# Kernel optimization log

Hardware: AMD Instinct MI355X
Metric: run time of the kernel (lower is better)

Reference implementation:

```python
import jax, jax.numpy as jnp
import numpy as np

H = 1024      # hidden_size
I = 2048      # expert intermediate_size (SwiGLU)
E = 8         # num_local_experts
B, S = 2, 4096
EPS = 1e-5
INIT = 0.02


def setup_inputs() -> dict:
    key = jax.random.key(0)
    ks = jax.random.split(key, 9)
    return {
        "hidden_states": jax.random.normal(ks[0], (B, S, H), jnp.float32),
        "ln_w": jnp.ones((H,), jnp.float32),
        "ln_b": jnp.zeros((H,), jnp.float32),
        "router_w": jax.random.normal(ks[1], (H, E), jnp.float32) * INIT,
        "gate_w": jax.random.normal(ks[2], (E, H, I), jnp.float32) * INIT,
        "up_w": jax.random.normal(ks[3], (E, H, I), jnp.float32) * INIT,
        "down_w": jax.random.normal(ks[4], (E, I, H), jnp.float32) * INIT,
        "sh_gate": jax.random.normal(ks[5], (H, I), jnp.float32) * INIT,
        "sh_up": jax.random.normal(ks[6], (H, I), jnp.float32) * INIT,
        "sh_down": jax.random.normal(ks[7], (I, H), jnp.float32) * INIT,
    }


def _layernorm(x, w, b):
    mu = jnp.mean(x, axis=-1, keepdims=True)
    var = jnp.mean(jnp.square(x - mu), axis=-1, keepdims=True)
    return (x - mu) * jax.lax.rsqrt(var + EPS) * w + b


def reference(hidden_states, ln_w, ln_b, router_w, gate_w, up_w, down_w,
              sh_gate, sh_up, sh_down):
    b, s, h = hidden_states.shape
    normed = _layernorm(hidden_states, ln_w, ln_b)
    xf = normed.reshape(-1, h)                       # [T, H]

    # Router: top-1 expert per token, sigmoid gating (Llama-4 style)
    logits = xf @ router_w                           # [T, E]
    top_idx = jnp.argmax(logits, axis=-1)            # [T]
    top_score = jax.nn.sigmoid(jnp.max(logits, axis=-1))  # [T]

    # Routed experts: scan over experts, mask+scale tokens assigned to each.
    def body(acc, ew):
        g, u, d, e = ew
        w = jnp.where(top_idx == e, top_score, 0.0)[:, None]  # [T, 1]
        xe = xf * w                                            # gate score applied to input
        hmid = jax.nn.silu(xe @ g) * (xe @ u)                  # [T, I]
        return acc + hmid @ d, None

    routed, _ = jax.lax.scan(
        body, jnp.zeros_like(xf), (gate_w, up_w, down_w, jnp.arange(E)))

    # Shared expert (dense SwiGLU) applied to all tokens
    shared = (jax.nn.silu(xf @ sh_gate) * (xf @ sh_up)) @ sh_down  # [T, H]

    moe_out = (routed + shared).reshape(b, s, h)
    return hidden_states + moe_out
```

## Files before the change

kernel.cpp:

```cpp
#include <hip/hip_runtime.h>

typedef unsigned short ushort_t;
typedef unsigned int uint_t;

#define T_TOK 8192
#define HDIM 1024
#define IDIM 2048
#define NEXP 8
#define RPAD_MAX 10240
#define TOTROWS (RPAD_MAX + T_TOK)

using f32x4 = __attribute__((ext_vector_type(4))) float;
using s16x8 = __attribute__((ext_vector_type(8))) short;

#define SBAR() do { asm volatile("" ::: "memory"); __builtin_amdgcn_s_barrier(); asm volatile("" ::: "memory"); } while (0)
#define VMW(n) asm volatile("s_waitcnt vmcnt(" #n ")" ::: "memory")
#define LGKM(n) do { asm volatile("s_waitcnt lgkmcnt(" #n ")" ::: "memory"); __builtin_amdgcn_sched_barrier(0); } while (0)

__device__ __forceinline__ float b2f(ushort_t h) {
    return __uint_as_float(((uint_t)h) << 16);
}
__device__ __forceinline__ ushort_t f2bf(float f) {
    uint_t u = __float_as_uint(f);
    uint_t r = (u + 0x7FFFu + ((u >> 16) & 1u)) >> 16;
    return (ushort_t)r;
}
__device__ __forceinline__ void gload16(const void* g, void* l) {
    __builtin_amdgcn_global_load_lds(
        (const __attribute__((address_space(1))) void*)g,
        (__attribute__((address_space(3))) void*)l, 16, 0, 0);
}
__device__ __forceinline__ void gdec(int gi, int& r, int& kg) {
    int prow = gi >> 3, v = (gi & 7) ^ (prow & 7);
    r = 2 * prow + (v >> 2);
    kg = v & 3;
}
__device__ __forceinline__ void sbmap(int bid, int SBC, int NSB, int& rt, int& ct) {
    int x = bid & 7, j = bid >> 3;
    int r = j >> 5, pos = j & 31;
    int sb = r * 8 + x;
    int rem = NSB - r * 8;
    if (rem < 8) {
        int share = 8 / rem;
        int cap = 32 / share;
        sb = r * 8 + x / share;
        pos = (x % share) * cap + (pos % cap);
    }
    int sbr = sb / SBC, sbc = sb % SBC;
    rt = sbr * 4 + (pos >> 3);
    ct = sbc * 8 + (pos & 7);
}

__global__ void tcvt64(const float* __restrict__ gw, const float* __restrict__ shg,
                       const float* __restrict__ uw, const float* __restrict__ shu,
                       const float* __restrict__ dw, const float* __restrict__ shd,
                       ushort_t* __restrict__ gwt, ushort_t* __restrict__ uwt,
                       ushort_t* __restrict__ dwt) {
    __shared__ float tile[64][65];
    int z = blockIdx.z;
    const float* src;
    ushort_t* dst;
    int R, C, bx = blockIdx.x, by = blockIdx.y;
    if (z < 18) {
        int zz = z % 9;
        R = HDIM; C = IDIM;
        if (z < 9) { src = zz < 8 ? gw + (size_t)zz * HDIM * IDIM : shg; dst = gwt + (size_t)zz * IDIM * HDIM; }
        else       { src = zz < 8 ? uw + (size_t)zz * HDIM * IDIM : shu; dst = uwt + (size_t)zz * IDIM * HDIM; }
    } else {
        int zz = z - 18;
        R = IDIM; C = HDIM;
        src = zz < 8 ? dw + (size_t)zz * IDIM * HDIM : shd;
        dst = dwt + (size_t)zz * HDIM * IDIM;
        int t = bx; bx = by; by = t;
    }
    int c0 = bx * 64, r0 = by * 64;
    int tx = threadIdx.x, ty = threadIdx.y;
#pragma unroll
    for (int i = 0; i < 16; ++i)
        tile[ty + i * 4][tx] = src[(size_t)(r0 + ty + i * 4) * C + c0 + tx];
    __syncthreads();
    int tid = ty * 64 + tx;
    int rr = (tid & 15) * 4, cc0 = tid >> 4;
#pragma unroll
    for (int it = 0; it < 4; ++it) {
        int c = cc0 + it * 16;
        ushort4 v;
        v.x = f2bf(tile[rr + 0][c]);
        v.y = f2bf(tile[rr + 1][c]);
        v.z = f2bf(tile[rr + 2][c]);
        v.w = f2bf(tile[rr + 3][c]);
        *(ushort4*)&dst[(size_t)(c0 + c) * R + r0 + rr] = v;
    }
}

__global__ void ln_router(const float* __restrict__ x, const float* __restrict__ lnw,
                          const float* __restrict__ lnb, const float* __restrict__ rw,
                          ushort_t* __restrict__ normed, int* __restrict__ top_idx,
                          float* __restrict__ top_score, int* __restrict__ cnt) {
    int t = blockIdx.x, tid = threadIdx.x;
    const float* xr = x + (size_t)t * HDIM;
    float v[4];
    float s = 0.f, ss = 0.f;
#pragma unroll
    for (int i = 0; i < 4; i++) {
        v[i] = xr[tid + i * 256];
        s += v[i];
        ss += v[i] * v[i];
    }
#pragma unroll
    for (int o = 32; o; o >>= 1) {
        s += __shfl_down(s, o);
        ss += __shfl_down(ss, o);
    }
    __shared__ float rs_[4], rss_[4], stats[2];
    int wid = tid >> 6, lane = tid & 63;
    if (!lane) { rs_[wid] = s; rss_[wid] = ss; }
    __syncthreads();
    if (!tid) {
        float S = rs_[0] + rs_[1] + rs_[2] + rs_[3];
        float SS = rss_[0] + rss_[1] + rss_[2] + rss_[3];
        float mu = S * (1.f / HDIM);
        float var = SS * (1.f / HDIM) - mu * mu;
        stats[0] = mu;
        stats[1] = rsqrtf(var + 1e-5f);
    }
    __syncthreads();
    float mu = stats[0], rsg = stats[1];
    float lg[8] = {0, 0, 0, 0, 0, 0, 0, 0};
#pragma unroll
    for (int i = 0; i < 4; i++) {
        int h = tid + i * 256;
        float xn = (v[i] - mu) * rsg * lnw[h] + lnb[h];
        normed[(size_t)t * HDIM + h] = f2bf(xn);
        const float* rwh = rw + (size_t)h * NEXP;
#pragma unroll
        for (int e = 0; e < 8; e++) lg[e] += xn * rwh[e];
    }
#pragma unroll
    for (int o = 32; o; o >>= 1)
#pragma unroll
        for (int e = 0; e < 8; e++) lg[e] += __shfl_down(lg[e], o);
    __shared__ float lred[4][8];
    if (!lane)
#pragma unroll
        for (int e = 0; e < 8; e++) lred[wid][e] = lg[e];
    __syncthreads();
    if (!tid) {
        float best = -1e30f;
        int bi = 0;
#pragma unroll
        for (int e = 0; e < 8; e++) {
            float L = lred[0][e] + lred[1][e] + lred[2][e] + lred[3][e];
            if (L > best) { best = L; bi = e; }
        }
        top_idx[t] = bi;
        top_score[t] = 1.f / (1.f + __expf(-best));
        atomicAdd(&cnt[bi], 1);
    }
}

__global__ void scan_k(const int* __restrict__ cnt, int* __restrict__ pad_off,
                       int* __restrict__ fill) {
    if (threadIdx.x == 0) {
        int o = 0;
        for (int e = 0; e < NEXP; e++) {
            pad_off[e] = o;
            o += (cnt[e] + 255) & ~255;
        }
        pad_off[NEXP] = o;
    }
    if (threadIdx.x < NEXP) fill[threadIdx.x] = 0;
}

__global__ void scatter_k(const ushort_t* __restrict__ normed, const int* __restrict__ top_idx,
                          const float* __restrict__ top_score, const int* __restrict__ pad_off,
                          int* __restrict__ fill, int* __restrict__ order,
                          ushort_t* __restrict__ xs) {
    int t = blockIdx.x, tid = threadIdx.x;
    __shared__ int spos;
    if (!tid) {
        int e = top_idx[t];
        int p = pad_off[e] + atomicAdd(&fill[e], 1);
        order[p] = t;
        spos = p;
    }
    __syncthreads();
    int pos = spos;
    float sc = top_score[t];
    const ushort4* src = (const ushort4*)(normed + (size_t)t * HDIM);
    ushort4* dst = (ushort4*)(xs + (size_t)pos * HDIM);
    ushort4 a = src[tid];
    a.x = f2bf(b2f(a.x) * sc);
    a.y = f2bf(b2f(a.y) * sc);
    a.z = f2bf(b2f(a.z) * sc);
    a.w = f2bf(b2f(a.w) * sc);
    dst[tid] = a;
}

__global__ __launch_bounds__(512, 2) void gemm1_k(
    const ushort_t* __restrict__ X, const ushort_t* __restrict__ Wg,
    const ushort_t* __restrict__ Wu, const int* __restrict__ pad_off,
    ushort_t* __restrict__ hmid) {
    __shared__ __align__(16) ushort_t lds[4 * 16384];
    const int CT = IDIM / 128;
    const int NH = HDIM / 32;
    int rt, ct;
    sbmap(blockIdx.x, CT / 8, (TOTROWS / 256 / 4) * (CT / 8), rt, ct);
    int row0 = rt * 256, col0 = ct * 128;
    int e;
    if (row0 >= RPAD_MAX) e = 8;
    else {
        if (row0 >= pad_off[NEXP]) return;
        e = 0;
        while (e < 7 && row0 >= pad_off[e + 1]) ++e;
    }
    const ushort_t* wgp = Wg + (size_t)e * IDIM * HDIM;
    const ushort_t* wup = Wu + (size_t)e * IDIM * HDIM;

    const int tid = threadIdx.x, l = tid & 63, w = tid >> 6;
    const int wm = w >> 2, wn = w & 3;
    const int lr = l & 15, lg4 = l >> 4;

    int rA0, kA0, rA1, kA1, rB, kB;
    gdec(tid, rA0, kA0);
    gdec(512 + tid, rA1, kA1);
    gdec(tid, rB, kB);
    const ushort_t* srcA0 = X + (size_t)(row0 + rA0) * HDIM + kA0 * 8;
    const ushort_t* srcA1 = X + (size_t)(row0 + rA1) * HDIM + kA1 * 8;
    const ushort_t* srcBg = wgp + (size_t)(col0 + rB) * HDIM + kB * 8;
    const ushort_t* srcBu = wup + (size_t)(col0 + rB) * HDIM + kB * 8;
    const int dA0 = tid * 8, dA1 = (512 + tid) * 8, dB = tid * 8;

    const int s_slot = (((l & 1) << 2) | lg4) ^ ((l >> 1) & 7);
    const int aoff = (wm * 64 + (lr >> 1)) * 64 + s_slot * 8;
    const int boff = (wn * 16 + (lr >> 1)) * 64 + s_slot * 8;

    f32x4 accg[8][2] = {};
    f32x4 accu[8][2] = {};

#define G1_STAGE(h) do { int ko = (h) * 32; int hb_ = ((h) & 3) * 16384;       \
        gload16(srcA0 + ko, &lds[hb_ + dA0]);                                  \
        gload16(srcA1 + ko, &lds[hb_ + dA1]);                                  \
        gload16(srcBg + ko, &lds[hb_ + 8192 + dB]);                            \
        gload16(srcBu + ko, &lds[hb_ + 12288 + dB]); } while (0)

#define G1_PH(h, VMWAIT, DOSTAGE) do {                                         \
        const int hb = ((h) & 3) * 16384;                                      \
        s16x8 av[8], bv[4];                                                    \
        _Pragma("unroll")                                                      \
        for (int i = 0; i < 4; ++i) av[i] = *(const s16x8*)&lds[hb + aoff + i * 512]; \
        _Pragma("unroll")                                                      \
        for (int i = 0; i < 2; ++i) bv[i] = *(const s16x8*)&lds[hb + 8192 + boff + i * 512]; \
        _Pragma("unroll")                                                      \
        for (int i = 0; i < 2; ++i) bv[2 + i] = *(const s16x8*)&lds[hb + 12288 + boff + i * 512]; \
        _Pragma("unroll")                                                      \
        for (int i = 0; i < 4; ++i) av[4 + i] = *(const s16x8*)&lds[hb + aoff + 2048 + i * 512]; \
        if (DOSTAGE) G1_STAGE((h) + 3);                                        \
        VMWAIT;                                                                \
        SBAR();                                                                \
        LGKM(4);                                                               \
        __builtin_amdgcn_s_setprio(1);                                         \
        _Pragma("unroll")                                                      \
        for (int m = 0; m < 4; ++m) {                                          \
            accg[m][0] = __builtin_amdgcn_mfma_f32_16x16x32_bf16(av[m], bv[0], accg[m][0], 0, 0, 0); \
            accg[m][1] = __builtin_amdgcn_mfma_f32_16x16x32_bf16(av[m], bv[1], accg[m][1], 0, 0, 0); \
            accu[m][0] = __builtin_amdgcn_mfma_f32_16x16x32_bf16(av[m], bv[2], accu[m][0], 0, 0, 0); \
            accu[m][1] = __builtin_amdgcn_mfma_f32_16x16x32_bf16(av[m], bv[3], accu[m][1], 0, 0, 0); \
        }                                                                      \
        __builtin_amdgcn_s_setprio(0);                                         \
        LGKM(0);                                                               \
        __builtin_amdgcn_s_setprio(1);                                         \
        _Pragma("unroll")                                                      \
        for (int m = 0; m < 4; ++m) {                                          \
            accg[4 + m][0] = __builtin_amdgcn_mfma_f32_16x16x32_bf16(av[4 + m], bv[0], accg[4 + m][0], 0, 0, 0); \
            accg[4 + m][1] = __builtin_amdgcn_mfma_f32_16x16x32_bf16(av[4 + m], bv[1], accg[4 + m][1], 0, 0, 0); \
            accu[4 + m][0] = __builtin_amdgcn_mfma_f32_16x16x32_bf16(av[4 + m], bv[2], accu[4 + m][0], 0, 0, 0); \
            accu[4 + m][1] = __builtin_amdgcn_mfma_f32_16x16x32_bf16(av[4 + m], bv[3], accu[4 + m][1], 0, 0, 0); \
        }                                                                      \
        __builtin_amdgcn_s_setprio(0);                                         \
        SBAR();                                                                \
    } while (0)

    G1_STAGE(0);
    G1_STAGE(1);
    G1_STAGE(2);
    VMW(8);
    SBAR();
    for (int h = 0; h < NH - 3; ++h) G1_PH(h, VMW(8), 1);
    G1_PH(NH - 3, VMW(4), 0);
    G1_PH(NH - 2, VMW(0), 0);
    G1_PH(NH - 1, VMW(0), 0);

#pragma unroll
    for (int mf = 0; mf < 8; ++mf) {
        int row = row0 + wm * 128 + mf * 16 + lg4 * 4;
#pragma unroll
        for (int nf = 0; nf < 2; ++nf) {
            int col = col0 + wn * 32 + nf * 16 + lr;
#pragma unroll
            for (int rr = 0; rr < 4; ++rr) {
                float g = accg[mf][nf][rr], u = accu[mf][nf][rr];
                float val = g / (1.f + __expf(-g)) * u;
                hmid[(size_t)(row + rr) * IDIM + col] = f2bf(val);
            }
        }
    }
#undef G1_STAGE
#undef G1_PH
}

template <int SHARED>
__global__ __launch_bounds__(512, 2) void gemm2_k(
    const ushort_t* __restrict__ Hm, const ushort_t* __restrict__ Wd,
    const int* __restrict__ pad_off, const int* __restrict__ order,
    const float* __restrict__ hs, float* __restrict__ out, int RT) {
    __shared__ __align__(16) ushort_t lds[4 * 12288];
    const int CT = HDIM / 128;
    const int NH = IDIM / 32;
    int rt, ct;
    sbmap(blockIdx.x, 1, RT / 4, rt, ct);
    int row0 = rt * 256, col0 = ct * 128;
    const ushort_t* wdp;
    if (SHARED) {
        wdp = Wd + (size_t)8 * HDIM * IDIM;
    } else {
        if (row0 >= pad_off[NEXP]) return;
        int e = 0;
        while (e < 7 && row0 >= pad_off[e + 1]) ++e;
        wdp = Wd + (size_t)e * HDIM * IDIM;
    }
    const int tid = threadIdx.x, l = tid & 63, w = tid >> 6;
    const int wm = w >> 1, wn = w & 1;
    const int lr = l & 15, lg4 = l >> 4;

    int rA0, kA0, rA1, kA1, rB, kB;
    gdec(tid, rA0, kA0);
    gdec(512 + tid, rA1, kA1);
    gdec(tid, rB, kB);
    const ushort_t* srcA0 = Hm + (size_t)(row0 + rA0) * IDIM + kA0 * 8;
    const ushort_t* srcA1 = Hm + (size_t)(row0 + rA1) * IDIM + kA1 * 8;
    const ushort_t* srcB = wdp + (size_t)(col0 + rB) * IDIM + kB * 8;
    const int dA0 = tid * 8, dA1 = (512 + tid) * 8, dB = tid * 8;

    const int s_slot = (((l & 1) << 2) | lg4) ^ ((l >> 1) & 7);
    const int aoff = (wm * 32 + (lr >> 1)) * 64 + s_slot * 8;
    const int boff = (wn * 32 + (lr >> 1)) * 64 + s_slot * 8;

    f32x4 acc[4][4] = {};

#define G2_STAGE(h) do { int ko = (h) * 32; int hb_ = ((h) & 3) * 12288;       \
        gload16(srcA0 + ko, &lds[hb_ + dA0]);                                  \
        gload16(srcA1 + ko, &lds[hb_ + dA1]);                                  \
        gload16(srcB + ko, &lds[hb_ + 8192 + dB]); } while (0)

#define G2_PH(h, VMWAIT, DOSTAGE) do {                                         \
        const int hb = ((h) & 3) * 12288;                                      \
        s16x8 av[4], bv[4];                                                    \
        _Pragma("unroll")                                                      \
        for (int i = 0; i < 4; ++i) av[i] = *(const s16x8*)&lds[hb + aoff + i * 512]; \
        _Pragma("unroll")                                                      \
        for (int i = 0; i < 4; ++i) bv[i] = *(const s16x8*)&lds[hb + 8192 + boff + i * 512]; \
        if (DOSTAGE) G2_STAGE((h) + 3);                                        \
        VMWAIT;                                                                \
        SBAR();                                                                \
        LGKM(0);                                                               \
        __builtin_amdgcn_s_setprio(1);                                         \
        _Pragma("unroll")                                                      \
        for (int m = 0; m < 4; ++m)                                            \
            _Pragma("unroll")                                                  \
            for (int n = 0; n < 4; ++n)                                        \
                acc[m][n] = __builtin_amdgcn_mfma_f32_16x16x32_bf16(av[m], bv[n], acc[m][n], 0, 0, 0); \
        __builtin_amdgcn_s_setprio(0);                                         \
        SBAR();                                                                \
    } while (0)

    G2_STAGE(0);
    G2_STAGE(1);
    G2_STAGE(2);
    VMW(6);
    SBAR();
    for (int h = 0; h < NH - 3; ++h) G2_PH(h, VMW(6), 1);
    G2_PH(NH - 3, VMW(3), 0);
    G2_PH(NH - 2, VMW(0), 0);
    G2_PH(NH - 1, VMW(0), 0);

#pragma unroll
    for (int mf = 0; mf < 4; ++mf) {
        int row = row0 + wm * 64 + mf * 16 + lg4 * 4;
#pragma unroll
        for (int nf = 0; nf < 4; ++nf) {
            int col = col0 + wn * 64 + nf * 16 + lr;
#pragma unroll
            for (int rr = 0; rr < 4; ++rr) {
                int rw_ = row + rr;
                if (SHARED) {
                    size_t o = (size_t)rw_ * HDIM + col;
                    out[o] += hs[o] + acc[mf][nf][rr];
                } else {
                    int tok = order[rw_];
                    if (tok >= 0) {
                        size_t o = (size_t)tok * HDIM + col;
                        out[o] = acc[mf][nf][rr];
                    }
                }
            }
        }
    }
#undef G2_STAGE
#undef G2_PH
}

extern "C" void kernel_launch(void* const* d_in, const int* in_sizes, int n_in,
                              void* d_out, int out_size, void* d_ws, size_t ws_size,
                              hipStream_t stream) {
    const float* hs = (const float*)d_in[0];
    const float* lnw = (const float*)d_in[1];
    const float* lnb = (const float*)d_in[2];
    const float* rw = (const float*)d_in[3];
    const float* gw = (const float*)d_in[4];
    const float* uw = (const float*)d_in[5];
    const float* dw = (const float*)d_in[6];
    const float* shg = (const float*)d_in[7];
    const float* shu = (const float*)d_in[8];
    const float* shd = (const float*)d_in[9];
    float* out = (float*)d_out;

    char* p = (char*)d_ws;
    auto alloc = [&](size_t bytes) {
        void* r = (void*)p;
        p += (bytes + 255) & ~(size_t)255;
        return r;
    };
    ushort_t* xsbuf = (ushort_t*)alloc((size_t)TOTROWS * HDIM * 2);
    ushort_t* hmid = (ushort_t*)alloc((size_t)TOTROWS * IDIM * 2);
    ushort_t* gwt = (ushort_t*)alloc((size_t)9 * IDIM * HDIM * 2);
    ushort_t* uwt = (ushort_t*)alloc((size_t)9 * IDIM * HDIM * 2);
    ushort_t* dwt = (ushort_t*)alloc((size_t)9 * HDIM * IDIM * 2);
    int* cnt = (int*)alloc(NEXP * 4);
    int* pad_off = (int*)alloc((NEXP + 1) * 4);
    int* fill = (int*)alloc(NEXP * 4);
    int* top_idx = (int*)alloc(T_TOK * 4);
    float* top_sc = (float*)alloc(T_TOK * 4);
    int* order = (int*)alloc(RPAD_MAX * 4);

    ushort_t* normed = xsbuf + (size_t)RPAD_MAX * HDIM;

    hipMemsetAsync(cnt, 0, NEXP * 4, stream);
    hipMemsetAsync(order, 0xFF, RPAD_MAX * 4, stream);
    hipMemsetAsync(xsbuf, 0, (size_t)RPAD_MAX * HDIM * 2, stream);

    tcvt64<<<dim3(IDIM / 64, HDIM / 64, 27), dim3(64, 4), 0, stream>>>(
        gw, shg, uw, shu, dw, shd, gwt, uwt, dwt);

    ln_router<<<T_TOK, 256, 0, stream>>>(hs, lnw, lnb, rw, normed, top_idx, top_sc, cnt);
    scan_k<<<1, 64, 0, stream>>>(cnt, pad_off, fill);
    scatter_k<<<T_TOK, 256, 0, stream>>>(normed, top_idx, top_sc, pad_off, fill, order, xsbuf);

    {
        int RT = TOTROWS / 256, CT = IDIM / 128;
        gemm1_k<<<RT * CT, 512, 0, stream>>>(xsbuf, gwt, uwt, pad_off, hmid);
    }
    {
        int RT = RPAD_MAX / 256;
        gemm2_k<0><<<RT * (HDIM / 128), 512, 0, stream>>>(
            hmid, dwt, pad_off, order, hs, out, RT);
    }
    {
        int RT = T_TOK / 256;
        gemm2_k<1><<<RT * (HDIM / 128), 512, 0, stream>>>(
            hmid + (size_t)RPAD_MAX * IDIM, dwt, pad_off, order, hs, out, RT);
    }
}
```

Baseline: 577.6 us.

## Switch expert GEMMs to BK=64 double-buffered LDS pipeline

```diff
diff --git a/kernel.cpp b/kernel.cpp
--- a/kernel.cpp
+++ b/kernel.cpp
@@ -16,6 +16,7 @@
 #define SBAR() do { asm volatile("" ::: "memory"); __builtin_amdgcn_s_barrier(); asm volatile("" ::: "memory"); } while (0)
 #define VMW(n) asm volatile("s_waitcnt vmcnt(" #n ")" ::: "memory")
 #define LGKM(n) do { asm volatile("s_waitcnt lgkmcnt(" #n ")" ::: "memory"); __builtin_amdgcn_sched_barrier(0); } while (0)
+#define SCHB() __builtin_amdgcn_sched_barrier(0)
 
 __device__ __forceinline__ float b2f(ushort_t h) {
     return __uint_as_float(((uint_t)h) << 16);
@@ -29,11 +30,6 @@
     __builtin_amdgcn_global_load_lds(
         (const __attribute__((address_space(1))) void*)g,
         (__attribute__((address_space(3))) void*)l, 16, 0, 0);
-}
-__device__ __forceinline__ void gdec(int gi, int& r, int& kg) {
-    int prow = gi >> 3, v = (gi & 7) ^ (prow & 7);
-    r = 2 * prow + (v >> 2);
-    kg = v & 3;
 }
 __device__ __forceinline__ void sbmap(int bid, int SBC, int NSB, int& rt, int& ct) {
     int x = bid & 7, j = bid >> 3;
@@ -201,9 +197,9 @@
     const ushort_t* __restrict__ X, const ushort_t* __restrict__ Wg,
     const ushort_t* __restrict__ Wu, const int* __restrict__ pad_off,
     ushort_t* __restrict__ hmid) {
-    __shared__ __align__(16) ushort_t lds[4 * 16384];
+    __shared__ __align__(16) ushort_t lds[2 * 32768];
     const int CT = IDIM / 128;
-    const int NH = HDIM / 32;
+    const int NH = HDIM / 64;
     int rt, ct;
     sbmap(blockIdx.x, CT / 8, (TOTROWS / 256 / 4) * (CT / 8), rt, ct);
     int row0 = rt * 256, col0 = ct * 128;
@@ -221,75 +217,85 @@
     const int wm = w >> 2, wn = w & 3;
     const int lr = l & 15, lg4 = l >> 4;
 
-    int rA0, kA0, rA1, kA1, rB, kB;
-    gdec(tid, rA0, kA0);
-    gdec(512 + tid, rA1, kA1);
-    gdec(tid, rB, kB);
-    const ushort_t* srcA0 = X + (size_t)(row0 + rA0) * HDIM + kA0 * 8;
-    const ushort_t* srcA1 = X + (size_t)(row0 + rA1) * HDIM + kA1 * 8;
-    const ushort_t* srcBg = wgp + (size_t)(col0 + rB) * HDIM + kB * 8;
-    const ushort_t* srcBu = wup + (size_t)(col0 + rB) * HDIM + kB * 8;
-    const int dA0 = tid * 8, dA1 = (512 + tid) * 8, dB = tid * 8;
-
-    const int s_slot = (((l & 1) << 2) | lg4) ^ ((l >> 1) & 7);
-    const int aoff = (wm * 64 + (lr >> 1)) * 64 + s_slot * 8;
-    const int boff = (wn * 16 + (lr >> 1)) * 64 + s_slot * 8;
+    const ushort_t* sA[4];
+#pragma unroll
+    for (int j = 0; j < 4; ++j) {
+        int gi = tid + j * 512, row = gi >> 3, kg = (gi & 7) ^ (row & 7);
+        sA[j] = X + (size_t)(row0 + row) * HDIM + kg * 8;
+    }
+    const ushort_t *sBg[2], *sBu[2];
+#pragma unroll
+    for (int j = 0; j < 2; ++j) {
+        int gi = tid + j * 512, row = gi >> 3, kg = (gi & 7) ^ (row & 7);
+        sBg[j] = wgp + (size_t)(col0 + row) * HDIM + kg * 8;
+        sBu[j] = wup + (size_t)(col0 + row) * HDIM + kg * 8;
+    }
+    const int sl0 = (lg4 ^ (lr & 7)) * 8, sl1 = ((4 + lg4) ^ (lr & 7)) * 8;
+    const int aob = (wm * 128 + lr) * 64;
+    const int bob = (wn * 32 + lr) * 64;
 
     f32x4 accg[8][2] = {};
     f32x4 accu[8][2] = {};
 
-#define G1_STAGE(h) do { int ko = (h) * 32; int hb_ = ((h) & 3) * 16384;       \
-        gload16(srcA0 + ko, &lds[hb_ + dA0]);                                  \
-        gload16(srcA1 + ko, &lds[hb_ + dA1]);                                  \
-        gload16(srcBg + ko, &lds[hb_ + 8192 + dB]);                            \
-        gload16(srcBu + ko, &lds[hb_ + 12288 + dB]); } while (0)
-
-#define G1_PH(h, VMWAIT, DOSTAGE) do {                                         \
-        const int hb = ((h) & 3) * 16384;                                      \
-        s16x8 av[8], bv[4];                                                    \
-        _Pragma("unroll")                                                      \
-        for (int i = 0; i < 4; ++i) av[i] = *(const s16x8*)&lds[hb + aoff + i * 512]; \
-        _Pragma("unroll")                                                      \
-        for (int i = 0; i < 2; ++i) bv[i] = *(const s16x8*)&lds[hb + 8192 + boff + i * 512]; \
-        _Pragma("unroll")                                                      \
-        for (int i = 0; i < 2; ++i) bv[2 + i] = *(const s16x8*)&lds[hb + 12288 + boff + i * 512]; \
-        _Pragma("unroll")                                                      \
-        for (int i = 0; i < 4; ++i) av[4 + i] = *(const s16x8*)&lds[hb + aoff + 2048 + i * 512]; \
-        if (DOSTAGE) G1_STAGE((h) + 3);                                        \
-        VMWAIT;                                                                \
-        SBAR();                                                                \
-        LGKM(4);                                                               \
+#define G1_STAGE(h) do { int ko = (h) * 64; int hb_ = ((h) & 1) * 32768;       \
+        gload16(sA[0] + ko, &lds[hb_ + tid * 8]);                              \
+        gload16(sA[1] + ko, &lds[hb_ + 4096 + tid * 8]);                       \
+        gload16(sA[2] + ko, &lds[hb_ + 8192 + tid * 8]);                       \
+        gload16(sA[3] + ko, &lds[hb_ + 12288 + tid * 8]);                      \
+        gload16(sBg[0] + ko, &lds[hb_ + 16384 + tid * 8]);                     \
+        gload16(sBg[1] + ko, &lds[hb_ + 20480 + tid * 8]);                     \
+        gload16(sBu[0] + ko, &lds[hb_ + 24576 + tid * 8]);                     \
+        gload16(sBu[1] + ko, &lds[hb_ + 28672 + tid * 8]); } while (0)
+
+#define G1_PH(h, DOSTAGE) do {                                                 \
+        const int hb = ((h) & 1) * 32768;                                      \
+        s16x8 a0[8], a1[8], b0[4], b1[4];                                      \
+        _Pragma("unroll")                                                      \
+        for (int m = 0; m < 8; ++m) a0[m] = *(const s16x8*)&lds[hb + aob + m * 1024 + sl0]; \
+        _Pragma("unroll")                                                      \
+        for (int n = 0; n < 2; ++n) {                                          \
+            b0[n] = *(const s16x8*)&lds[hb + 16384 + bob + n * 1024 + sl0];    \
+            b0[2 + n] = *(const s16x8*)&lds[hb + 24576 + bob + n * 1024 + sl0]; \
+        }                                                                      \
+        SCHB();                                                                \
+        _Pragma("unroll")                                                      \
+        for (int m = 0; m < 8; ++m) a1[m] = *(const s16x8*)&lds[hb + aob + m * 1024 + sl1]; \
+        _Pragma("unroll")                                                      \
+        for (int n = 0; n < 2; ++n) {                                          \
+            b1[n] = *(const s16x8*)&lds[hb + 16384 + bob + n * 1024 + sl1];    \
+            b1[2 + n] = *(const s16x8*)&lds[hb + 24576 + bob + n * 1024 + sl1]; \
+        }                                                                      \
+        SCHB();                                                                \
+        if (DOSTAGE) G1_STAGE((h) + 1);                                        \
+        LGKM(12);                                                              \
         __builtin_amdgcn_s_setprio(1);                                         \
         _Pragma("unroll")                                                      \
-        for (int m = 0; m < 4; ++m) {                                          \
-            accg[m][0] = __builtin_amdgcn_mfma_f32_16x16x32_bf16(av[m], bv[0], accg[m][0], 0, 0, 0); \
-            accg[m][1] = __builtin_amdgcn_mfma_f32_16x16x32_bf16(av[m], bv[1], accg[m][1], 0, 0, 0); \
-            accu[m][0] = __builtin_amdgcn_mfma_f32_16x16x32_bf16(av[m], bv[2], accu[m][0], 0, 0, 0); \
-            accu[m][1] = __builtin_amdgcn_mfma_f32_16x16x32_bf16(av[m], bv[3], accu[m][1], 0, 0, 0); \
+        for (int m = 0; m < 8; ++m) {                                          \
+            accg[m][0] = __builtin_amdgcn_mfma_f32_16x16x32_bf16(a0[m], b0[0], accg[m][0], 0, 0, 0); \
+            accg[m][1] = __builtin_amdgcn_mfma_f32_16x16x32_bf16(a0[m], b0[1], accg[m][1], 0, 0, 0); \
+            accu[m][0] = __builtin_amdgcn_mfma_f32_16x16x32_bf16(a0[m], b0[2], accu[m][0], 0, 0, 0); \
+            accu[m][1] = __builtin_amdgcn_mfma_f32_16x16x32_bf16(a0[m], b0[3], accu[m][1], 0, 0, 0); \
         }                                                                      \
         __builtin_amdgcn_s_setprio(0);                                         \
         LGKM(0);                                                               \
         __builtin_amdgcn_s_setprio(1);                                         \
         _Pragma("unroll")                                                      \
-        for (int m = 0; m < 4; ++m) {                                          \
-            accg[4 + m][0] = __builtin_amdgcn_mfma_f32_16x16x32_bf16(av[4 + m], bv[0], accg[4 + m][0], 0, 0, 0); \
-            accg[4 + m][1] = __builtin_amdgcn_mfma_f32_16x16x32_bf16(av[4 + m], bv[1], accg[4 + m][1], 0, 0, 0); \
-            accu[4 + m][0] = __builtin_amdgcn_mfma_f32_16x16x32_bf16(av[4 + m], bv[2], accu[4 + m][0], 0, 0, 0); \
-            accu[4 + m][1] = __builtin_amdgcn_mfma_f32_16x16x32_bf16(av[4 + m], bv[3], accu[4 + m][1], 0, 0, 0); \
+        for (int m = 0; m < 8; ++m) {                                          \
+            accg[m][0] = __builtin_amdgcn_mfma_f32_16x16x32_bf16(a1[m], b1[0], accg[m][0], 0, 0, 0); \
+            accg[m][1] = __builtin_amdgcn_mfma_f32_16x16x32_bf16(a1[m], b1[1], accg[m][1], 0, 0, 0); \
+            accu[m][0] = __builtin_amdgcn_mfma_f32_16x16x32_bf16(a1[m], b1[2], accu[m][0], 0, 0, 0); \
+            accu[m][1] = __builtin_amdgcn_mfma_f32_16x16x32_bf16(a1[m], b1[3], accu[m][1], 0, 0, 0); \
         }                                                                      \
         __builtin_amdgcn_s_setprio(0);                                         \
+        VMW(0);                                                                \
         SBAR();                                                                \
     } while (0)
 
     G1_STAGE(0);
-    G1_STAGE(1);
-    G1_STAGE(2);
-    VMW(8);
+    VMW(0);
     SBAR();
-    for (int h = 0; h < NH - 3; ++h) G1_PH(h, VMW(8), 1);
-    G1_PH(NH - 3, VMW(4), 0);
-    G1_PH(NH - 2, VMW(0), 0);
-    G1_PH(NH - 1, VMW(0), 0);
+    for (int h = 0; h < NH - 1; ++h) G1_PH(h, 1);
+    G1_PH(NH - 1, 0);
 
 #pragma unroll
     for (int mf = 0; mf < 8; ++mf) {
@@ -314,9 +320,8 @@
     const ushort_t* __restrict__ Hm, const ushort_t* __restrict__ Wd,
     const int* __restrict__ pad_off, const int* __restrict__ order,
     const float* __restrict__ hs, float* __restrict__ out, int RT) {
-    __shared__ __align__(16) ushort_t lds[4 * 12288];
-    const int CT = HDIM / 128;
-    const int NH = IDIM / 32;
+    __shared__ __align__(16) ushort_t lds[2 * 24576];
+    const int NH = IDIM / 64;
     int rt, ct;
     sbmap(blockIdx.x, 1, RT / 4, rt, ct);
     int row0 = rt * 256, col0 = ct * 128;
@@ -333,56 +338,71 @@
     const int wm = w >> 1, wn = w & 1;
     const int lr = l & 15, lg4 = l >> 4;
 
-    int rA0, kA0, rA1, kA1, rB, kB;
-    gdec(tid, rA0, kA0);
-    gdec(512 + tid, rA1, kA1);
-    gdec(tid, rB, kB);
-    const ushort_t* srcA0 = Hm + (size_t)(row0 + rA0) * IDIM + kA0 * 8;
-    const ushort_t* srcA1 = Hm + (size_t)(row0 + rA1) * IDIM + kA1 * 8;
-    const ushort_t* srcB = wdp + (size_t)(col0 + rB) * IDIM + kB * 8;
-    const int dA0 = tid * 8, dA1 = (512 + tid) * 8, dB = tid * 8;
-
-    const int s_slot = (((l & 1) << 2) | lg4) ^ ((l >> 1) & 7);
-    const int aoff = (wm * 32 + (lr >> 1)) * 64 + s_slot * 8;
-    const int boff = (wn * 32 + (lr >> 1)) * 64 + s_slot * 8;
+    const ushort_t* sA[4];
+#pragma unroll
+    for (int j = 0; j < 4; ++j) {
+        int gi = tid + j * 512, row = gi >> 3, kg = (gi & 7) ^ (row & 7);
+        sA[j] = Hm + (size_t)(row0 + row) * IDIM + kg * 8;
+    }
+    const ushort_t* sB[2];
+#pragma unroll
+    for (int j = 0; j < 2; ++j) {
+        int gi = tid + j * 512, row = gi >> 3, kg = (gi & 7) ^ (row & 7);
+        sB[j] = wdp + (size_t)(col0 + row) * IDIM + kg * 8;
+    }
+    const int sl0 = (lg4 ^ (lr & 7)) * 8, sl1 = ((4 + lg4) ^ (lr & 7)) * 8;
+    const int aob = (wm * 64 + lr) * 64;
+    const int bob = (wn * 64 + lr) * 64;
 
     f32x4 acc[4][4] = {};
 
-#define G2_STAGE(h) do { int ko = (h) * 32; int hb_ = ((h) & 3) * 12288;       \
-        gload16(srcA0 + ko, &lds[hb_ + dA0]);                                  \
-        gload16(srcA1 + ko, &lds[hb_ + dA1]);                                  \
-        gload16(srcB + ko, &lds[hb_ + 8192 + dB]); } while (0)
-
-#define G2_PH(h, VMWAIT, DOSTAGE) do {                                         \
-        const int hb = ((h) & 3) * 12288;                                      \
-        s16x8 av[4], bv[4];                                                    \
-        _Pragma("unroll")                                                      \
-        for (int i = 0; i < 4; ++i) av[i] = *(const s16x8*)&lds[hb + aoff + i * 512]; \
-        _Pragma("unroll")                                                      \
-        for (int i = 0; i < 4; ++i) bv[i] = *(const s16x8*)&lds[hb + 8192 + boff + i * 512]; \
-        if (DOSTAGE) G2_STAGE((h) + 3);                                        \
-        VMWAIT;                                                                \
-        SBAR();                                                                \
-        LGKM(0);                                                               \
+#define G2_STAGE(h) do { int ko = (h) * 64; int hb_ = ((h) & 1) * 24576;       \
+        gload16(sA[0] + ko, &lds[hb_ + tid * 8]);                              \
+        gload16(sA[1] + ko, &lds[hb_ + 4096 + tid * 8]);                       \
+        gload16(sA[2] + ko, &lds[hb_ + 8192 + tid * 8]);                       \
+        gload16(sA[3] + ko, &lds[hb_ + 12288 + tid * 8]);                      \
+        gload16(sB[0] + ko, &lds[hb_ + 16384 + tid * 8]);                      \
+        gload16(sB[1] + ko, &lds[hb_ + 20480 + tid * 8]); } while (0)
+
+#define G2_PH(h, DOSTAGE) do {                                                 \
+        const int hb = ((h) & 1) * 24576;                                      \
+        s16x8 a0[4], a1[4], b0[4], b1[4];                                      \
+        _Pragma("unroll")                                                      \
+        for (int m = 0; m < 4; ++m) a0[m] = *(const s16x8*)&lds[hb + aob + m * 1024 + sl0]; \
+        _Pragma("unroll")                                                      \
+        for (int n = 0; n < 4; ++n) b0[n] = *(const s16x8*)&lds[hb + 16384 + bob + n * 1024 + sl0]; \
+        SCHB();                                                                \
+        _Pragma("unroll")                                                      \
+        for (int m = 0; m < 4; ++m) a1[m] = *(const s16x8*)&lds[hb + aob + m * 1024 + sl1]; \
+        _Pragma("unroll")                                                      \
+        for (int n = 0; n < 4; ++n) b1[n] = *(const s16x8*)&lds[hb + 16384 + bob + n * 1024 + sl1]; \
+        SCHB();                                                                \
+        if (DOSTAGE) G2_STAGE((h) + 1);                                        \
+        LGKM(8);                                                               \
         __builtin_amdgcn_s_setprio(1);                                         \
         _Pragma("unroll")                                                      \
         for (int m = 0; m < 4; ++m)                                            \
             _Pragma("unroll")                                                  \
             for (int n = 0; n < 4; ++n)                                        \
-                acc[m][n] = __builtin_amdgcn_mfma_f32_16x16x32_bf16(av[m], bv[n], acc[m][n], 0, 0, 0); \
+                acc[m][n] = __builtin_amdgcn_mfma_f32_16x16x32_bf16(a0[m], b0[n], acc[m][n], 0, 0, 0); \
         __builtin_amdgcn_s_setprio(0);                                         \
+        LGKM(0);                                                               \
+        __builtin_amdgcn_s_setprio(1);                                         \
+        _Pragma("unroll")                                                      \
+        for (int m = 0; m < 4; ++m)                                            \
+            _Pragma("unroll")                                                  \
+            for (int n = 0; n < 4; ++n)                                        \
+                acc[m][n] = __builtin_amdgcn_mfma_f32_16x16x32_bf16(a1[m], b1[n], acc[m][n], 0, 0, 0); \
+        __builtin_amdgcn_s_setprio(0);                                         \
+        VMW(0);                                                                \
         SBAR();                                                                \
     } while (0)
 
     G2_STAGE(0);
-    G2_STAGE(1);
-    G2_STAGE(2);
-    VMW(6);
+    VMW(0);
     SBAR();
-    for (int h = 0; h < NH - 3; ++h) G2_PH(h, VMW(6), 1);
-    G2_PH(NH - 3, VMW(3), 0);
-    G2_PH(NH - 2, VMW(0), 0);
-    G2_PH(NH - 1, VMW(0), 0);
+    for (int h = 0; h < NH - 1; ++h) G2_PH(h, 1);
+    G2_PH(NH - 1, 0);
 
 #pragma unroll
     for (int mf = 0; mf < 4; ++mf) {
```

Measured after the change: 563.7 us. 2.4% less time.
